# Kernel tuning notes

Measured on AMD Instinct MI355X. Metric: run time of the kernel, lower is better.

Reference implementation:

```python
import jax, jax.numpy as jnp
import numpy as np

DIM = 96       # d_model / channels
DSTATE = 16    # SSM state size N
DINNER = 2 * DIM   # expand=2 -> 192
DTRANK = 6     # ceil(DIM/16)
K = 4          # scan directions
B, H, W = 2, 56, 56


def _ln(x, g, b, eps=1e-5):
    m = x.mean(-1, keepdims=True)
    v = x.var(-1, keepdims=True)
    return (x - m) * jax.lax.rsqrt(v + eps) * g + b


def _dwconv3(x, w, b):  # x [B,C,H,W], w [C,1,3,3] depthwise, SAME padding
    y = jax.lax.conv_general_dilated(x, w, (1, 1), [(1, 1), (1, 1)],
                                     feature_group_count=x.shape[1],
                                     dimension_numbers=('NCHW', 'OIHW', 'NCHW'))
    return y + b[None, :, None, None]


def _bn(x, g, b, m, v, eps=1e-5):  # eval-mode BatchNorm2d on NCHW
    inv = jax.lax.rsqrt(v + eps)
    return (x - m[None, :, None, None]) * (inv * g)[None, :, None, None] + b[None, :, None, None]


def _selective_scan(u, dt, A, Bs, Cs, Dp, dt_bias):
    # u, dt: [B,K,D,L]; A: [K,D,N]; Bs,Cs: [B,K,N,L]; Dp, dt_bias: [K,D]
    dt = jax.nn.softplus(dt + dt_bias[None, :, :, None])
    dA = jnp.exp(jnp.einsum('bkdl,kdn->lbkdn', dt, A))           # [L,B,K,D,N]
    dBu = jnp.einsum('bkdl,bknl,bkdl->lbkdn', dt, Bs, u)          # [L,B,K,D,N]
    Ct = jnp.moveaxis(Cs, -1, 0)                                  # [L,B,K,N]
    h0 = jnp.zeros(dA.shape[1:], dA.dtype)

    def step(h, inp):
        dA_l, dBu_l, C_l = inp
        h = dA_l * h + dBu_l
        return h, jnp.einsum('bkdn,bkn->bkd', h, C_l)

    _, ys = jax.lax.scan(step, h0, (dA, dBu, Ct))                 # ys [L,B,K,D]
    return jnp.moveaxis(ys, 0, -1) + u * Dp[None, :, :, None]     # [B,K,D,L]


def setup_inputs() -> dict:
    key = jax.random.key(0)
    ks = jax.random.split(key, 12)
    s = 0.02
    f32 = jnp.float32
    inp = {}
    inp['x'] = jax.random.normal(ks[0], (B, H, W, DIM), f32)
    # conv branch: depthwise 3x3 + BN + ReLU + 1x1 + BN
    inp['dw_w'] = jax.random.normal(ks[1], (DIM, 1, 3, 3), f32) * s
    inp['dw_b'] = jnp.zeros((DIM,), f32)
    inp['bn1_g'] = jnp.ones((DIM,), f32); inp['bn1_b'] = jnp.zeros((DIM,), f32)
    inp['bn1_m'] = jnp.zeros((DIM,), f32); inp['bn1_v'] = jnp.ones((DIM,), f32)
    inp['pw_w'] = jax.random.normal(ks[2], (DIM, DIM), f32) * s
    inp['pw_b'] = jnp.zeros((DIM,), f32)
    inp['bn2_g'] = jnp.ones((DIM,), f32); inp['bn2_b'] = jnp.zeros((DIM,), f32)
    inp['bn2_m'] = jnp.zeros((DIM,), f32); inp['bn2_v'] = jnp.ones((DIM,), f32)
    # pre-mamba LayerNorm
    inp['ln_g'] = jnp.ones((DIM,), f32); inp['ln_b'] = jnp.zeros((DIM,), f32)
    # SS2D params
    inp['in_proj_w'] = jax.random.normal(ks[3], (2 * DINNER, DIM), f32) * s
    inp['conv_w'] = jax.random.normal(ks[4], (DINNER, 1, 3, 3), f32) * s
    inp['conv_b'] = jnp.zeros((DINNER,), f32)
    inp['x_proj_w'] = jax.random.normal(ks[5], (K, DTRANK + 2 * DSTATE, DINNER), f32) * s
    inp['dt_w'] = jax.random.normal(ks[6], (K, DINNER, DTRANK), f32) * s
    inp['dt_b'] = jnp.full((K, DINNER), -4.6, f32)  # softplus(dt_b) ~= 0.01
    inp['A_logs'] = jnp.log(jnp.tile(jnp.arange(1, DSTATE + 1, dtype=f32), (K * DINNER, 1)))
    inp['Ds'] = jnp.ones((K * DINNER,), f32)
    inp['out_norm_g'] = jnp.ones((DINNER,), f32); inp['out_norm_b'] = jnp.zeros((DINNER,), f32)
    inp['out_proj_w'] = jax.random.normal(ks[7], (DIM, DINNER), f32) * s
    # fusion: Linear(2*dim, dim) + LayerNorm(dim)
    inp['fus_w'] = jax.random.normal(ks[8], (DIM, 2 * DIM), f32) * s
    inp['fus_b'] = jnp.zeros((DIM,), f32)
    inp['fus_ln_g'] = jnp.ones((DIM,), f32); inp['fus_ln_b'] = jnp.zeros((DIM,), f32)
    return inp


def reference(x, dw_w, dw_b, bn1_g, bn1_b, bn1_m, bn1_v, pw_w, pw_b,
              bn2_g, bn2_b, bn2_m, bn2_v, ln_g, ln_b,
              in_proj_w, conv_w, conv_b, x_proj_w, dt_w, dt_b, A_logs, Ds,
              out_norm_g, out_norm_b, out_proj_w, fus_w, fus_b, fus_ln_g, fus_ln_b):
    Bsz, Hh, Ww, C = x.shape
    L = Hh * Ww
    # ----- conv branch -----
    xc = jnp.transpose(x, (0, 3, 1, 2))                       # [B,C,H,W]
    c = jax.nn.relu(_bn(_dwconv3(xc, dw_w, dw_b), bn1_g, bn1_b, bn1_m, bn1_v))
    c = jnp.einsum('bchw,oc->bohw', c, pw_w) + pw_b[None, :, None, None]
    conv_out = jnp.transpose(_bn(c, bn2_g, bn2_b, bn2_m, bn2_v), (0, 2, 3, 1))
    # ----- mamba (SS2D) branch -----
    xn = _ln(x, ln_g, ln_b)
    xz = xn @ in_proj_w.T                                     # [B,H,W,2*Din]
    xm, z = jnp.split(xz, 2, axis=-1)
    xm = jnp.transpose(xm, (0, 3, 1, 2))                      # [B,Din,H,W]
    xm = jax.nn.silu(_dwconv3(xm, conv_w, conv_b))
    v1 = xm.reshape(Bsz, DINNER, L)                           # row-major scan
    v2 = jnp.transpose(xm, (0, 1, 3, 2)).reshape(Bsz, DINNER, L)  # col-major scan
    xs = jnp.stack([v1, v2, v1[..., ::-1], v2[..., ::-1]], axis=1)  # [B,4,Din,L]
    x_dbl = jnp.einsum('bkdl,kcd->bkcl', xs, x_proj_w)
    dts, Bmat, Cmat = jnp.split(x_dbl, [DTRANK, DTRANK + DSTATE], axis=2)
    dts = jnp.einsum('bkrl,kdr->bkdl', dts, dt_w)
    A = -jnp.exp(A_logs).reshape(K, DINNER, DSTATE)
    out_y = _selective_scan(xs, dts, A, Bmat, Cmat, Ds.reshape(K, DINNER), dt_b)
    y1 = out_y[:, 0]
    inv_y = out_y[:, 2:4][..., ::-1]
    y2 = inv_y[:, 0]
    y3 = jnp.transpose(inv_y[:, 1].reshape(Bsz, DINNER, Ww, Hh), (0, 1, 3, 2)).reshape(Bsz, DINNER, L)
    y4 = jnp.transpose(out_y[:, 1].reshape(Bsz, DINNER, Ww, Hh), (0, 1, 3, 2)).reshape(Bsz, DINNER, L)
    y = jnp.transpose(y1 + y2 + y3 + y4, (0, 2, 1)).reshape(Bsz, Hh, Ww, DINNER)
    y = _ln(y, out_norm_g, out_norm_b)
    y = y * jax.nn.silu(z)
    mamba_out = y @ out_proj_w.T                              # [B,H,W,C]
    # ----- fusion + residual -----
    fused = jnp.concatenate([conv_out, mamba_out], axis=-1) @ fus_w.T + fus_b
    fused = _ln(fused, fus_ln_g, fus_ln_b)
    return x + fused
```

## Files before the change

kernel.cpp:

```cpp
#include <hip/hip_runtime.h>
#include <math.h>

#define BZ 2
#define HH 56
#define WW 56
#define LL 3136
#define CC 96
#define DI 192
#define NS 16
#define RR 6
#define NT 49
#define NCH 98
#define CH 32

#define OFF_CONV   0
#define OFF_XMRAW  602112
#define OFF_Z      1806336
#define OFF_V1     3010560
#define OFF_V2     4214784
#define OFF_DT     5419008
#define OFF_BS     10235904
#define OFF_CS     10637312
#define OFF_Y      11038720
#define OFF_Y13    15855616
#define OFF_T      18264064
#define OFF_W2     19468288

__device__ __forceinline__ float softplusf(float x) {
    if (x > 20.f) return x;
    return log1pf(__expf(x));
}

__global__ __launch_bounds__(64) void k0_w2(const float* __restrict__ fus_w,
                                            const float* __restrict__ opw,
                                            float* __restrict__ W2) {
    int i = blockIdx.x * 64 + threadIdx.x;
    if (i >= CC * DI) return;
    int o = i / DI, d = i % DI;
    float acc = 0.f;
    for (int j = 0; j < CC; ++j)
        acc += fus_w[o * DI + CC + j] * opw[j * DI + d];
    W2[i] = acc;
}

__global__ __launch_bounds__(256) void k0c_negA(const float* __restrict__ A_logs,
                                                float* __restrict__ negA) {
    int i = blockIdx.x * 256 + threadIdx.x;
    if (i < 4 * DI * NS) negA[i] = -__expf(A_logs[i]);
}

__global__ __launch_bounds__(256) void k1a_dw(const float* __restrict__ x,
    const float* __restrict__ dw_w, const float* __restrict__ dw_b,
    const float* __restrict__ bn1_g, const float* __restrict__ bn1_b,
    const float* __restrict__ bn1_m, const float* __restrict__ bn1_v,
    float* __restrict__ cbuf) {
    int i = blockIdx.x * 256 + threadIdx.x;
    if (i >= BZ * LL * CC) return;
    int c = i % CC;
    int bl = i / CC;
    int l = bl % LL, b = bl / LL;
    int h = l / WW, w = l % WW;
    float acc = dw_b[c];
    #pragma unroll
    for (int dy = -1; dy <= 1; ++dy) {
        int hh = h + dy; if (hh < 0 || hh >= HH) continue;
        #pragma unroll
        for (int dx = -1; dx <= 1; ++dx) {
            int ww = w + dx; if (ww < 0 || ww >= WW) continue;
            acc += x[((b * HH + hh) * WW + ww) * CC + c] * dw_w[c * 9 + (dy + 1) * 3 + (dx + 1)];
        }
    }
    float inv = rsqrtf(bn1_v[c] + 1e-5f);
    float v = (acc - bn1_m[c]) * inv * bn1_g[c] + bn1_b[c];
    cbuf[i] = fmaxf(v, 0.f);
}

__global__ __launch_bounds__(256) void k1b_pw(const float* __restrict__ cbuf,
    const float* __restrict__ pw_w, const float* __restrict__ pw_b,
    const float* __restrict__ bn2_g, const float* __restrict__ bn2_b,
    const float* __restrict__ bn2_m, const float* __restrict__ bn2_v,
    float* __restrict__ conv_out) {
    int t0 = blockIdx.x * 64;
    int og = blockIdx.y;
    int b = blockIdx.z;
    int lane = threadIdx.x & 63;
    int wvu = __builtin_amdgcn_readfirstlane(threadIdx.x >> 6);
    __shared__ float ct[CC * 65];
    __shared__ float res[64 * 49];
    const float* cb = cbuf + (b * LL + t0) * CC;
    for (int e = threadIdx.x; e < 64 * CC; e += 256) {
        int p = e / CC, c = e % CC;
        ct[c * 65 + p] = cb[e];
    }
    __syncthreads();
    int o0 = og * 48 + wvu * 12;
    float acc[12];
    const float* pb = pw_b + o0;
    #pragma unroll
    for (int j = 0; j < 12; ++j) acc[j] = pb[j];
    const float* wb = pw_w + o0 * CC;
    for (int c = 0; c < CC; ++c) {
        float xv = ct[c * 65 + lane];
        #pragma unroll
        for (int j = 0; j < 12; ++j)
            acc[j] += xv * wb[j * CC + c];
    }
    #pragma unroll
    for (int j = 0; j < 12; ++j) {
        int o = o0 + j;
        float inv = rsqrtf(bn2_v[o] + 1e-5f);
        res[lane * 49 + wvu * 12 + j] = (acc[j] - bn2_m[o]) * inv * bn2_g[o] + bn2_b[o];
    }
    __syncthreads();
    float* ob = conv_out + (b * LL + t0) * CC + og * 48;
    for (int e = threadIdx.x; e < 64 * 48; e += 256) {
        int pl = e / 48, o = e % 48;
        ob[pl * CC + o] = res[pl * 49 + o];
    }
}

__global__ __launch_bounds__(256) void k2_inproj(const float* __restrict__ x,
    const float* __restrict__ ln_g, const float* __restrict__ ln_b,
    const float* __restrict__ ipw,
    float* __restrict__ xm_raw, float* __restrict__ z_buf) {
    int t0 = blockIdx.x * 64;
    int og = blockIdx.y;
    int b = blockIdx.z;
    int lane = threadIdx.x & 63;
    int wv = threadIdx.x >> 6;
    int wvu = __builtin_amdgcn_readfirstlane(wv);
    __shared__ float xt[64 * 97];
    __shared__ float xn[96 * 65];
    __shared__ float ps[4][64], ps2[4][64];
    const float* xb = x + (b * LL + t0) * CC;
    for (int e = threadIdx.x; e < 64 * CC; e += 256) {
        int p = e / CC, c = e % CC;
        xt[p * 97 + c] = xb[e];
    }
    __syncthreads();
    float s = 0.f, s2 = 0.f;
    #pragma unroll
    for (int j = 0; j < 24; ++j) {
        float v = xt[lane * 97 + wvu * 24 + j];
        s += v; s2 += v * v;
    }
    ps[wv][lane] = s; ps2[wv][lane] = s2;
    __syncthreads();
    float st = 0.f, st2 = 0.f;
    #pragma unroll
    for (int i = 0; i < 4; ++i) { st += ps[i][lane]; st2 += ps2[i][lane]; }
    float m = st * (1.f / 96.f);
    float inv = rsqrtf(st2 * (1.f / 96.f) - m * m + 1e-5f);
    #pragma unroll
    for (int j = 0; j < 24; ++j) {
        int c = wvu * 24 + j;
        xn[c * 65 + lane] = (xt[lane * 97 + c] - m) * inv * ln_g[c] + ln_b[c];
    }
    __syncthreads();
    float acc[12];
    #pragma unroll
    for (int j = 0; j < 12; ++j) acc[j] = 0.f;
    int o0 = og * 48 + wvu * 12;
    const float* wbase = ipw + o0 * CC;
    for (int c = 0; c < CC; ++c) {
        float xv = xn[c * 65 + lane];
        #pragma unroll
        for (int j = 0; j < 12; ++j)
            acc[j] += xv * wbase[j * CC + c];
    }
    int p = t0 + lane;
    #pragma unroll
    for (int j = 0; j < 12; ++j) {
        int out = o0 + j;
        if (out < DI) xm_raw[(b * DI + out) * LL + p] = acc[j];
        else          z_buf[(b * DI + (out - DI)) * LL + p] = acc[j];
    }
}

__global__ __launch_bounds__(256) void k3_dw(const float* __restrict__ xm_raw,
    const float* __restrict__ conv_w, const float* __restrict__ conv_b,
    float* __restrict__ v1, float* __restrict__ v2) {
    int bd = blockIdx.x;
    int half = blockIdx.y;
    int d = bd % DI;
    int h0 = half * 28;
    __shared__ float tile[28 * 57];
    const float* src = xm_raw + bd * LL;
    float wloc[9];
    #pragma unroll
    for (int i = 0; i < 9; ++i) wloc[i] = conv_w[d * 9 + i];
    float bias = conv_b[d];
    for (int e = threadIdx.x; e < 28 * WW; e += 256) {
        int hl = e / WW, w = e % WW;
        int h = h0 + hl;
        float acc = bias;
        #pragma unroll
        for (int dy = -1; dy <= 1; ++dy) {
            int hh = h + dy; if (hh < 0 || hh >= HH) continue;
            #pragma unroll
            for (int dx = -1; dx <= 1; ++dx) {
                int ww = w + dx; if (ww < 0 || ww >= WW) continue;
                acc += src[hh * WW + ww] * wloc[(dy + 1) * 3 + (dx + 1)];
            }
        }
        float sig = 1.f / (1.f + __expf(-acc));
        float v = acc * sig;
        v1[bd * LL + h * WW + w] = v;
        tile[hl * 57 + w] = v;
    }
    __syncthreads();
    for (int e = threadIdx.x; e < 28 * WW; e += 256) {
        int w = e / 28, hl = e % 28;
        v2[bd * LL + w * HH + h0 + hl] = tile[hl * 57 + w];
    }
}

__global__ __launch_bounds__(256) void k4a_xproj(const float* __restrict__ v1,
    const float* __restrict__ v2, const float* __restrict__ xpw,
    float* __restrict__ dtr_g, float* __restrict__ B_s, float* __restrict__ C_s) {
    int tile = blockIdx.x;
    int k = blockIdx.y, b = blockIdx.z;
    int lane = threadIdx.x & 63;
    int wvu = __builtin_amdgcn_readfirstlane(threadIdx.x >> 6);
    int t0 = tile * 64;
    int r0 = wvu * 10; if (r0 > 28) r0 = 28;
    const float* src = ((k & 1) == 0 ? v1 : v2) + b * DI * LL + t0;
    float acc[10];
    #pragma unroll
    for (int i = 0; i < 10; ++i) acc[i] = 0.f;
    const float* wbase = xpw + (k * 38 + r0) * DI;
    for (int d = 0; d < DI; ++d) {
        float xv = src[d * LL + lane];
        #pragma unroll
        for (int i = 0; i < 10; ++i)
            acc[i] += xv * wbase[i * DI + d];
    }
    int bk = b * 4 + k;
    int p = t0 + lane;
    #pragma unroll
    for (int i = 0; i < 10; ++i) {
        int c = r0 + i;
        if (c < RR) {
            dtr_g[(bk * RR + c) * LL + p] = acc[i];
        } else if (c < RR + NS) {
            B_s[(bk * NS + (c - RR)) * LL + p] = acc[i];
        } else {
            C_s[(bk * NS + (c - RR - NS)) * LL + p] = acc[i];
        }
    }
}

__global__ __launch_bounds__(256) void k4b_dt(const float* __restrict__ dtr_g,
    const float* __restrict__ dtw, const float* __restrict__ dtb,
    float* __restrict__ dt_s) {
    int t0 = blockIdx.x * 64;
    int k = blockIdx.y, b = blockIdx.z;
    int lane = threadIdx.x & 63;
    int wvu = __builtin_amdgcn_readfirstlane(threadIdx.x >> 6);
    int bk = b * 4 + k;
    int p = t0 + lane;
    float r[RR];
    #pragma unroll
    for (int i = 0; i < RR; ++i) r[i] = dtr_g[(bk * RR + i) * LL + p];
    for (int i = 0; i < 48; ++i) {
        int d = wvu * 48 + i;
        float a = dtb[k * DI + d];
        const float* wr = dtw + (k * DI + d) * RR;
        #pragma unroll
        for (int q = 0; q < RR; ++q)
            a += r[q] * wr[q];
        dt_s[(bk * DI + d) * LL + p] = softplusf(a);
    }
}

__global__ __launch_bounds__(128, 4) void k5a_scan(const float* __restrict__ dt_s,
    const float* __restrict__ B_s, const float* __restrict__ C_s,
    const float* __restrict__ v1, const float* __restrict__ v2,
    const float* __restrict__ A_logs, float* __restrict__ y_scan,
    float* __restrict__ hl_buf, float* __restrict__ Tbuf) {
    int bx = blockIdx.x;
    int dg = bx % 3, c = bx / 3;
    int k = blockIdx.y, b = blockIdx.z;
    int bk = b * 4 + k;
    int tid = threadIdx.x;
    int lane = tid & 63;
    int wvu = __builtin_amdgcn_readfirstlane(tid >> 6);
    int d0 = dg * 64, d = d0 + lane;
    bool fwd = (k < 2);
    int s0 = fwd ? c * CH : (LL - (c + 1) * CH);
    __shared__ float dtl[64 * 32];
    __shared__ float ul[64 * 32];
    __shared__ alignas(16) float bc[32 * 32];
    float Ae[8];
    const float* ap = A_logs + (k * DI + d) * NS + wvu * 8;
    #pragma unroll
    for (int n = 0; n < 8; ++n) Ae[n] = -__expf(ap[n]) * 1.442695040888963f;
    const float* dtp = dt_s + (bk * DI + d0) * LL + s0;
    const float* up  = ((k & 1) == 0 ? v1 : v2) + (b * DI + d0) * LL + s0;
    #pragma unroll
    for (int q = 0; q < 4; ++q) {
        int e = q * 128 + tid;
        int row = e >> 3;
        int p4 = (e & 7) << 2;
        float4 dv = *(const float4*)(dtp + row * LL + p4);
        float4 uv = *(const float4*)(up + row * LL + p4);
        float dvv[4] = {dv.x, dv.y, dv.z, dv.w};
        float uvv[4] = {uv.x, uv.y, uv.z, uv.w};
        int rsw = row & 31;
        #pragma unroll
        for (int t = 0; t < 4; ++t) {
            int s = fwd ? (p4 + t) : (31 - (p4 + t));
            dtl[row * 32 + (s ^ rsw)] = dvv[t];
            ul [row * 32 + (s ^ rsw)] = dvv[t] * uvv[t];
        }
    }
    #pragma unroll
    for (int q = 0; q < 2; ++q) {
        int e = q * 128 + tid;
        int row = e >> 3;
        int p4 = (e & 7) << 2;
        const float* src = (row < 16 ? B_s + (bk * NS + row) * LL
                                     : C_s + (bk * NS + (row - 16)) * LL) + s0 + p4;
        float4 v = *(const float4*)src;
        float vv[4] = {v.x, v.y, v.z, v.w};
        #pragma unroll
        for (int t = 0; t < 4; ++t) {
            int s = fwd ? (p4 + t) : (31 - (p4 + t));
            bc[s * 32 + (row ^ ((s & 7) << 2))] = vv[t];
        }
    }
    __syncthreads();
    float h[8];
    #pragma unroll
    for (int n = 0; n < 8; ++n) h[n] = 0.f;
    float cum = 0.f;
    int lbase = lane * 32;
    int lsw = lane & 31;
    int w8 = wvu * 8;
    #pragma unroll
    for (int seg = 0; seg < 4; ++seg) {
        float yv_[8];
        #pragma unroll
        for (int jj = 0; jj < 8; ++jj) {
            int j = seg * 8 + jj;
            float dtv = dtl[lbase + (j ^ lsw)];
            float du  = ul [lbase + (j ^ lsw)];
            cum += dtv;
            int cswz = (j & 7) << 2;
            const float* rb0 = &bc[j * 32 + ( w8       ^ cswz)];
            const float* rb1 = &bc[j * 32 + ((w8 +  4) ^ cswz)];
            const float* rc0 = &bc[j * 32 + ((w8 + 16) ^ cswz)];
            const float* rc1 = &bc[j * 32 + ((w8 + 20) ^ cswz)];
            float4 b0 = *(const float4*)rb0, b1 = *(const float4*)rb1;
            float4 c0 = *(const float4*)rc0, c1 = *(const float4*)rc1;
            float bv[8] = {b0.x, b0.y, b0.z, b0.w, b1.x, b1.y, b1.z, b1.w};
            float cv[8] = {c0.x, c0.y, c0.z, c0.w, c1.x, c1.y, c1.z, c1.w};
            float y = 0.f;
            #pragma unroll
            for (int n = 0; n < 8; ++n) {
                h[n] = exp2f(dtv * Ae[n]) * h[n] + du * bv[n];
                y += h[n] * cv[n];
            }
            yv_[jj] = y;
        }
        __syncthreads();
        float* dst = (wvu == 0) ? dtl : ul;
        #pragma unroll
        for (int jj = 0; jj < 8; ++jj) {
            int j = seg * 8 + jj;
            dst[lbase + (j ^ lsw)] = yv_[jj];
        }
    }
    __syncthreads();
    float* yp = y_scan + (bk * DI + d0) * LL + s0;
    #pragma unroll
    for (int q = 0; q < 4; ++q) {
        int e = q * 128 + tid;
        int row = e >> 3;
        int p4 = (e & 7) << 2;
        int rsw = row & 31;
        float ov[4];
        #pragma unroll
        for (int t = 0; t < 4; ++t) {
            int s = fwd ? (p4 + t) : (31 - (p4 + t));
            ov[t] = dtl[row * 32 + (s ^ rsw)] + ul[row * 32 + (s ^ rsw)];
        }
        *(float4*)(yp + row * LL + p4) = make_float4(ov[0], ov[1], ov[2], ov[3]);
    }
    float4* hp4 = (float4*)(hl_buf + (bk * NCH + c) * (DI * NS) + d * NS + wvu * 8);
    hp4[0] = make_float4(h[0], h[1], h[2], h[3]);
    hp4[1] = make_float4(h[4], h[5], h[6], h[7]);
    if (wvu == 0) Tbuf[(bk * NCH + c) * DI + d] = cum;
}

__global__ __launch_bounds__(64) void k5c_comb(float* __restrict__ hl_buf,
    const float* __restrict__ Tbuf, const float* __restrict__ negA) {
    int dg = blockIdx.x, k = blockIdx.y, b = blockIdx.z;
    int lane = threadIdx.x, dl = lane >> 4, n = lane & 15;
    int d = dg * 4 + dl;
    int bk = b * 4 + k;
    float Av = negA[(k * DI + d) * NS + n];
    float H = 0.f;
    float* slot0 = hl_buf + (bk * NCH + 0) * (DI * NS) + dg * 64 + lane;
    float hl_next = *slot0;
    float T_next = Tbuf[(bk * NCH + 0) * DI + d];
    for (int c = 0; c < NCH; ++c) {
        float hl = hl_next, T = T_next;
        if (c + 1 < NCH) {
            hl_next = hl_buf[(bk * NCH + c + 1) * (DI * NS) + dg * 64 + lane];
            T_next  = Tbuf[(bk * NCH + c + 1) * DI + d];
        }
        hl_buf[(bk * NCH + c) * (DI * NS) + dg * 64 + lane] = H;
        H = hl + __expf(Av * T) * H;
    }
}

__global__ __launch_bounds__(256) void k5d_corr(const float* __restrict__ dt_s,
    const float* __restrict__ C_s, const float* __restrict__ hin,
    const float* __restrict__ negA, float* __restrict__ y_scan) {
    int t = blockIdx.x;
    int k = blockIdx.y, b = blockIdx.z;
    bool fwd = (k < 2);
    int c  = fwd ? (t + 1) : (NCH - 1 - t);
    int s0 = fwd ? (t + 1) * CH : t * CH;
    int p32 = threadIdx.x & 31, sl = threadIdx.x >> 5;
    int bk = b * 4 + k;
    __shared__ float c_l[16 * 33];
    for (int e = threadIdx.x; e < 16 * CH; e += 256) {
        int n = e >> 5, s = e & 31;
        c_l[n * 33 + s] = C_s[(bk * NS + n) * LL + s0 + s];
    }
    __syncthreads();
    for (int j = 0; j < 24; ++j) {
        int d = sl * 24 + j;
        float dtv = dt_s[(bk * DI + d) * LL + s0 + p32];
        float cum = dtv;
        if (fwd) {
            #pragma unroll
            for (int off = 1; off < 32; off <<= 1) {
                float o = __shfl_up(cum, off, 32);
                if (p32 >= off) cum += o;
            }
        } else {
            #pragma unroll
            for (int off = 1; off < 32; off <<= 1) {
                float o = __shfl_down(cum, off, 32);
                if (p32 < 32 - off) cum += o;
            }
        }
        const float* hp = hin + (bk * NCH + c) * (DI * NS) + d * 16;
        const float* ap = negA + (k * DI + d) * NS;
        float acc = 0.f;
        #pragma unroll
        for (int n = 0; n < 16; ++n) {
            acc += c_l[n * 33 + p32] * __expf(ap[n] * cum) * hp[n];
        }
        y_scan[(bk * DI + d) * LL + s0 + p32] += acc;
    }
}

__global__ __launch_bounds__(256) void k5b_tr(const float* __restrict__ y_scan,
                                              float* __restrict__ y13t) {
    int idx = blockIdx.x;
    int d = idx % DI;
    int bk = idx / DI;
    int kk = bk % 2, b = bk / 2;
    int k = (kk == 0) ? 1 : 3;
    __shared__ float tile[HH * 57];
    const float* src = y_scan + ((b * 4 + k) * DI + d) * LL;
    for (int e = threadIdx.x; e < LL; e += 256) {
        int w = e / HH, h = e % HH;
        tile[h * 57 + w] = src[e];
    }
    __syncthreads();
    float* dst = y13t + idx * LL;
    for (int e = threadIdx.x; e < LL; e += 256) {
        int h = e / WW, w = e % WW;
        dst[e] = tile[h * 57 + w];
    }
}

__global__ __launch_bounds__(256) void k6_gather(const float* __restrict__ y_scan,
    const float* __restrict__ y13t, const float* __restrict__ v1,
    const float* __restrict__ z_buf, const float* __restrict__ Ds,
    const float* __restrict__ ong, const float* __restrict__ onb,
    float* __restrict__ t_buf) {
    int t0 = blockIdx.x * 16;
    int b = blockIdx.y;
    int p16 = threadIdx.x & 15, sl = threadIdx.x >> 4;
    int p = t0 + p16;
    __shared__ float yv[DI * 17];
    __shared__ float ps[16][16], ps2[16][16];
    float s = 0.f, s2 = 0.f;
    for (int j = 0; j < 12; ++j) {
        int d = sl * 12 + j;
        float dsum = Ds[d] + Ds[DI + d] + Ds[2 * DI + d] + Ds[3 * DI + d];
        float val = y_scan[((b * 4 + 0) * DI + d) * LL + p]
                  + y_scan[((b * 4 + 2) * DI + d) * LL + p]
                  + y13t[((b * 2 + 0) * DI + d) * LL + p]
                  + y13t[((b * 2 + 1) * DI + d) * LL + p]
                  + v1[(b * DI + d) * LL + p] * dsum;
        yv[d * 17 + p16] = val;
        s += val; s2 += val * val;
    }
    ps[sl][p16] = s; ps2[sl][p16] = s2;
    __syncthreads();
    float st = 0.f, st2 = 0.f;
    #pragma unroll
    for (int i = 0; i < 16; ++i) { st += ps[i][p16]; st2 += ps2[i][p16]; }
    float m = st * (1.f / 192.f);
    float inv = rsqrtf(st2 * (1.f / 192.f) - m * m + 1e-5f);
    for (int j = 0; j < 12; ++j) {
        int d = sl * 12 + j;
        float val = (yv[d * 17 + p16] - m) * inv * ong[d] + onb[d];
        float zz = z_buf[(b * DI + d) * LL + p];
        float sig = 1.f / (1.f + __expf(-zz));
        t_buf[(b * DI + d) * LL + p] = val * zz * sig;
    }
}

__global__ __launch_bounds__(256) void k7a_mm(const float* __restrict__ t_buf,
    const float* __restrict__ conv_out, const float* __restrict__ W2,
    const float* __restrict__ fus_w, const float* __restrict__ fus_b,
    float* __restrict__ fusedT) {
    int t0 = blockIdx.x * 64;
    int og = blockIdx.y;
    int b = blockIdx.z;
    int lane = threadIdx.x & 63;
    int wvu = __builtin_amdgcn_readfirstlane(threadIdx.x >> 6);
    __shared__ float ct[CC * 65];
    const float* cb = conv_out + (b * LL + t0) * CC;
    for (int e = threadIdx.x; e < 64 * CC; e += 256) {
        int p = e / CC, c = e % CC;
        ct[c * 65 + p] = cb[e];
    }
    __syncthreads();
    int o0 = og * 12 + wvu * 3;
    float acc[3];
    #pragma unroll
    for (int j = 0; j < 3; ++j) acc[j] = fus_b[o0 + j];
    int p = t0 + lane;
    const float* w2 = W2 + o0 * DI;
    for (int d = 0; d < DI; ++d) {
        float tv = t_buf[(b * DI + d) * LL + p];
        #pragma unroll
        for (int j = 0; j < 3; ++j)
            acc[j] += tv * w2[j * DI + d];
    }
    const float* fw = fus_w + o0 * DI;
    for (int c = 0; c < CC; ++c) {
        float cv = ct[c * 65 + lane];
        #pragma unroll
        for (int j = 0; j < 3; ++j)
            acc[j] += cv * fw[j * DI + c];
    }
    #pragma unroll
    for (int j = 0; j < 3; ++j)
        fusedT[(b * CC + o0 + j) * LL + p] = acc[j];
}

__global__ __launch_bounds__(256) void k7b_ln(const float* __restrict__ fusedT,
    const float* __restrict__ flg, const float* __restrict__ flb,
    const float* __restrict__ x, float* __restrict__ out) {
    int t0 = blockIdx.x * 16;
    int b = blockIdx.y;
    int p16 = threadIdx.x & 15, sl = threadIdx.x >> 4;
    __shared__ float ft[CC * 17];
    __shared__ float res[16 * 97];
    __shared__ float ps[16][16], ps2[16][16];
    for (int e = threadIdx.x; e < CC * 16; e += 256) {
        int o = e >> 4, p = e & 15;
        ft[o * 17 + p] = fusedT[(b * CC + o) * LL + t0 + p];
    }
    __syncthreads();
    float s = 0.f, s2 = 0.f;
    #pragma unroll
    for (int j = 0; j < 6; ++j) {
        float v = ft[(sl * 6 + j) * 17 + p16];
        s += v; s2 += v * v;
    }
    ps[sl][p16] = s; ps2[sl][p16] = s2;
    __syncthreads();
    float st = 0.f, st2 = 0.f;
    #pragma unroll
    for (int i = 0; i < 16; ++i) { st += ps[i][p16]; st2 += ps2[i][p16]; }
    float m = st * (1.f / 96.f);
    float inv = rsqrtf(st2 * (1.f / 96.f) - m * m + 1e-5f);
    #pragma unroll
    for (int j = 0; j < 6; ++j) {
        int o = sl * 6 + j;
        res[p16 * 97 + o] = (ft[o * 17 + p16] - m) * inv * flg[o] + flb[o];
    }
    __syncthreads();
    const float* xb = x + (b * LL + t0) * CC;
    float* ob = out + (b * LL + t0) * CC;
    for (int e = threadIdx.x; e < 16 * CC; e += 256) {
        int pl = e / CC, o = e % CC;
        ob[e] = xb[e] + res[pl * 97 + o];
    }
}

extern "C" void kernel_launch(void* const* d_in, const int* in_sizes, int n_in,
                              void* d_out, int out_size, void* d_ws, size_t ws_size,
                              hipStream_t stream) {
    const float* x        = (const float*)d_in[0];
    const float* dw_w     = (const float*)d_in[1];
    const float* dw_b     = (const float*)d_in[2];
    const float* bn1_g    = (const float*)d_in[3];
    const float* bn1_b    = (const float*)d_in[4];
    const float* bn1_m    = (const float*)d_in[5];
    const float* bn1_v    = (const float*)d_in[6];
    const float* pw_w     = (const float*)d_in[7];
    const float* pw_b     = (const float*)d_in[8];
    const float* bn2_g    = (const float*)d_in[9];
    const float* bn2_b    = (const float*)d_in[10];
    const float* bn2_m    = (const float*)d_in[11];
    const float* bn2_v    = (const float*)d_in[12];
    const float* ln_g     = (const float*)d_in[13];
    const float* ln_b     = (const float*)d_in[14];
    const float* ipw      = (const float*)d_in[15];
    const float* conv_w   = (const float*)d_in[16];
    const float* conv_b   = (const float*)d_in[17];
    const float* xpw      = (const float*)d_in[18];
    const float* dtw      = (const float*)d_in[19];
    const float* dtb      = (const float*)d_in[20];
    const float* A_logs   = (const float*)d_in[21];
    const float* Ds       = (const float*)d_in[22];
    const float* ong      = (const float*)d_in[23];
    const float* onb      = (const float*)d_in[24];
    const float* opw      = (const float*)d_in[25];
    const float* fus_w    = (const float*)d_in[26];
    const float* fus_b    = (const float*)d_in[27];
    const float* flg      = (const float*)d_in[28];
    const float* flb      = (const float*)d_in[29];

    float* ws = (float*)d_ws;
    float* conv_out = ws + OFF_CONV;
    float* xm_raw   = ws + OFF_XMRAW;
    float* z_buf    = ws + OFF_Z;
    float* v1       = ws + OFF_V1;
    float* v2       = ws + OFF_V2;
    float* dt_s     = ws + OFF_DT;
    float* B_s      = ws + OFF_BS;
    float* C_s      = ws + OFF_CS;
    float* y_scan   = ws + OFF_Y;
    float* y13t     = ws + OFF_Y13;
    float* t_buf    = ws + OFF_T;
    float* W2       = ws + OFF_W2;
    float* cbuf     = y13t;
    float* hl_buf   = y13t;
    float* Tbuf     = xm_raw;
    float* dtr_g    = xm_raw + 262144;
    float* negA     = B_s;
    float* fusedT   = y13t;
    float* out      = (float*)d_out;

    k0_w2<<<dim3((CC * DI + 63) / 64), dim3(64), 0, stream>>>(fus_w, opw, W2);
    k1a_dw<<<dim3((BZ * LL * CC + 255) / 256), dim3(256), 0, stream>>>(x, dw_w, dw_b,
                                                     bn1_g, bn1_b, bn1_m, bn1_v, cbuf);
    k1b_pw<<<dim3(NT, 2, BZ), dim3(256), 0, stream>>>(cbuf, pw_w, pw_b,
                                                   bn2_g, bn2_b, bn2_m, bn2_v, conv_out);
    k2_inproj<<<dim3(NT, 8, BZ), dim3(256), 0, stream>>>(x, ln_g, ln_b, ipw, xm_raw, z_buf);
    k3_dw<<<dim3(BZ * DI, 2), dim3(256), 0, stream>>>(xm_raw, conv_w, conv_b, v1, v2);
    k4a_xproj<<<dim3(NT, 4, BZ), dim3(256), 0, stream>>>(v1, v2, xpw, dtr_g, B_s, C_s);
    k4b_dt<<<dim3(NT, 4, BZ), dim3(256), 0, stream>>>(dtr_g, dtw, dtb, dt_s);
    k5a_scan<<<dim3(3 * NCH, 4, BZ), dim3(128), 0, stream>>>(dt_s, B_s, C_s, v1, v2, A_logs,
                                                             y_scan, hl_buf, Tbuf);
    k0c_negA<<<dim3(48), dim3(256), 0, stream>>>(A_logs, negA);
    k5c_comb<<<dim3(48, 4, BZ), dim3(64), 0, stream>>>(hl_buf, Tbuf, negA);
    k5d_corr<<<dim3(NCH - 1, 4, BZ), dim3(256), 0, stream>>>(dt_s, C_s, hl_buf, negA, y_scan);
    k5b_tr<<<dim3(BZ * 2 * DI), dim3(256), 0, stream>>>(y_scan, y13t);
    k6_gather<<<dim3(196, BZ), dim3(256), 0, stream>>>(y_scan, y13t, v1, z_buf, Ds, ong, onb, t_buf);
    k7a_mm<<<dim3(NT, 8, BZ), dim3(256), 0, stream>>>(t_buf, conv_out, W2, fus_w, fus_b, fusedT);
    k7b_ln<<<dim3(196, BZ), dim3(256), 0, stream>>>(fusedT, flg, flb, x, out);
}
```

Baseline: 357.2 us.

## Fuse dt projection and softplus into scan and correction kernels

Removes the separate dt kernel and its 2x4x192x3136 dt_s buffer. The scan and correction kernels now rebuild dt from the rank-6 projection on the fly (6 FMAs plus softplus per element), cutting a large global write and two reads. The combine kernel also gains an 8-deep software prefetch of chunk states to hide load latency on its serial chain. The cost is that dt is computed twice, and the scan kernel's prologue carries more arithmetic and register pressure.

```diff
diff --git a/kernel.cpp b/kernel.cpp
--- a/kernel.cpp
+++ b/kernel.cpp
@@ -250,30 +250,8 @@
     }
 }
 
-__global__ __launch_bounds__(256) void k4b_dt(const float* __restrict__ dtr_g,
+__global__ __launch_bounds__(128, 4) void k5a_scan(const float* __restrict__ dtr_g,
     const float* __restrict__ dtw, const float* __restrict__ dtb,
-    float* __restrict__ dt_s) {
-    int t0 = blockIdx.x * 64;
-    int k = blockIdx.y, b = blockIdx.z;
-    int lane = threadIdx.x & 63;
-    int wvu = __builtin_amdgcn_readfirstlane(threadIdx.x >> 6);
-    int bk = b * 4 + k;
-    int p = t0 + lane;
-    float r[RR];
-    #pragma unroll
-    for (int i = 0; i < RR; ++i) r[i] = dtr_g[(bk * RR + i) * LL + p];
-    for (int i = 0; i < 48; ++i) {
-        int d = wvu * 48 + i;
-        float a = dtb[k * DI + d];
-        const float* wr = dtw + (k * DI + d) * RR;
-        #pragma unroll
-        for (int q = 0; q < RR; ++q)
-            a += r[q] * wr[q];
-        dt_s[(bk * DI + d) * LL + p] = softplusf(a);
-    }
-}
-
-__global__ __launch_bounds__(128, 4) void k5a_scan(const float* __restrict__ dt_s,
     const float* __restrict__ B_s, const float* __restrict__ C_s,
     const float* __restrict__ v1, const float* __restrict__ v2,
     const float* __restrict__ A_logs, float* __restrict__ y_scan,
@@ -291,44 +269,62 @@
     __shared__ float dtl[64 * 32];
     __shared__ float ul[64 * 32];
     __shared__ alignas(16) float bc[32 * 32];
-    float Ae[8];
-    const float* ap = A_logs + (k * DI + d) * NS + wvu * 8;
-    #pragma unroll
-    for (int n = 0; n < 8; ++n) Ae[n] = -__expf(ap[n]) * 1.442695040888963f;
-    const float* dtp = dt_s + (bk * DI + d0) * LL + s0;
     const float* up  = ((k & 1) == 0 ? v1 : v2) + (b * DI + d0) * LL + s0;
+    int p4 = (tid & 7) << 2;
+    int row0 = tid >> 3;
+    const float* dtrp = dtr_g + (bk * RR) * LL + s0 + p4;
+    float4 rv0 = *(const float4*)(dtrp + 0 * LL);
+    float4 rv1 = *(const float4*)(dtrp + 1 * LL);
+    float4 rv2 = *(const float4*)(dtrp + 2 * LL);
+    float4 rv3 = *(const float4*)(dtrp + 3 * LL);
+    float4 rv4 = *(const float4*)(dtrp + 4 * LL);
+    float4 rv5 = *(const float4*)(dtrp + 5 * LL);
     #pragma unroll
     for (int q = 0; q < 4; ++q) {
-        int e = q * 128 + tid;
-        int row = e >> 3;
-        int p4 = (e & 7) << 2;
-        float4 dv = *(const float4*)(dtp + row * LL + p4);
+        int row = row0 + 16 * q;
+        int dd = k * DI + d0 + row;
+        const float* wr = dtw + dd * RR;
+        float2 w01 = *(const float2*)(wr);
+        float2 w23 = *(const float2*)(wr + 2);
+        float2 w45 = *(const float2*)(wr + 4);
+        float bias = dtb[dd];
+        float a0 = bias, a1 = bias, a2 = bias, a3 = bias;
+        a0 += rv0.x * w01.x; a1 += rv0.y * w01.x; a2 += rv0.z * w01.x; a3 += rv0.w * w01.x;
+        a0 += rv1.x * w01.y; a1 += rv1.y * w01.y; a2 += rv1.z * w01.y; a3 += rv1.w * w01.y;
+        a0 += rv2.x * w23.x; a1 += rv2.y * w23.x; a2 += rv2.z * w23.x; a3 += rv2.w * w23.x;
+        a0 += rv3.x * w23.y; a1 += rv3.y * w23.y; a2 += rv3.z * w23.y; a3 += rv3.w * w23.y;
+        a0 += rv4.x * w45.x; a1 += rv4.y * w45.x; a2 += rv4.z * w45.x; a3 += rv4.w * w45.x;
+        a0 += rv5.x * w45.y; a1 += rv5.y * w45.y; a2 += rv5.z * w45.y; a3 += rv5.w * w45.y;
+        float dts[4] = {softplusf(a0), softplusf(a1), softplusf(a2), softplusf(a3)};
         float4 uv = *(const float4*)(up + row * LL + p4);
-        float dvv[4] = {dv.x, dv.y, dv.z, dv.w};
         float uvv[4] = {uv.x, uv.y, uv.z, uv.w};
         int rsw = row & 31;
         #pragma unroll
         for (int t = 0; t < 4; ++t) {
             int s = fwd ? (p4 + t) : (31 - (p4 + t));
-            dtl[row * 32 + (s ^ rsw)] = dvv[t];
-            ul [row * 32 + (s ^ rsw)] = dvv[t] * uvv[t];
+            dtl[row * 32 + (s ^ rsw)] = dts[t];
+            ul [row * 32 + (s ^ rsw)] = dts[t] * uvv[t];
         }
     }
     #pragma unroll
     for (int q = 0; q < 2; ++q) {
         int e = q * 128 + tid;
         int row = e >> 3;
-        int p4 = (e & 7) << 2;
+        int pp4 = (e & 7) << 2;
         const float* src = (row < 16 ? B_s + (bk * NS + row) * LL
-                                     : C_s + (bk * NS + (row - 16)) * LL) + s0 + p4;
+                                     : C_s + (bk * NS + (row - 16)) * LL) + s0 + pp4;
         float4 v = *(const float4*)src;
         float vv[4] = {v.x, v.y, v.z, v.w};
         #pragma unroll
         for (int t = 0; t < 4; ++t) {
-            int s = fwd ? (p4 + t) : (31 - (p4 + t));
+            int s = fwd ? (pp4 + t) : (31 - (pp4 + t));
             bc[s * 32 + (row ^ ((s & 7) << 2))] = vv[t];
         }
     }
+    float Ae[8];
+    const float* ap = A_logs + (k * DI + d) * NS + wvu * 8;
+    #pragma unroll
+    for (int n = 0; n < 8; ++n) Ae[n] = -__expf(ap[n]) * 1.442695040888963f;
     __syncthreads();
     float h[8];
     #pragma unroll
@@ -377,15 +373,15 @@
     for (int q = 0; q < 4; ++q) {
         int e = q * 128 + tid;
         int row = e >> 3;
-        int p4 = (e & 7) << 2;
+        int pp4 = (e & 7) << 2;
         int rsw = row & 31;
         float ov[4];
         #pragma unroll
         for (int t = 0; t < 4; ++t) {
-            int s = fwd ? (p4 + t) : (31 - (p4 + t));
+            int s = fwd ? (pp4 + t) : (31 - (pp4 + t));
             ov[t] = dtl[row * 32 + (s ^ rsw)] + ul[row * 32 + (s ^ rsw)];
         }
-        *(float4*)(yp + row * LL + p4) = make_float4(ov[0], ov[1], ov[2], ov[3]);
+        *(float4*)(yp + row * LL + pp4) = make_float4(ov[0], ov[1], ov[2], ov[3]);
     }
     float4* hp4 = (float4*)(hl_buf + (bk * NCH + c) * (DI * NS) + d * NS + wvu * 8);
     hp4[0] = make_float4(h[0], h[1], h[2], h[3]);
@@ -399,23 +395,32 @@
     int lane = threadIdx.x, dl = lane >> 4, n = lane & 15;
     int d = dg * 4 + dl;
     int bk = b * 4 + k;
+    const int HS = DI * NS;
     float Av = negA[(k * DI + d) * NS + n];
+    float* hp = hl_buf + (bk * NCH) * HS + dg * 64 + lane;
+    const float* Tp = Tbuf + (bk * NCH) * DI + d;
+    float hl[8], T[8];
+    #pragma unroll
+    for (int i = 0; i < 8; ++i) { hl[i] = hp[i * HS]; T[i] = Tp[i * DI]; }
     float H = 0.f;
-    float* slot0 = hl_buf + (bk * NCH + 0) * (DI * NS) + dg * 64 + lane;
-    float hl_next = *slot0;
-    float T_next = Tbuf[(bk * NCH + 0) * DI + d];
-    for (int c = 0; c < NCH; ++c) {
-        float hl = hl_next, T = T_next;
-        if (c + 1 < NCH) {
-            hl_next = hl_buf[(bk * NCH + c + 1) * (DI * NS) + dg * 64 + lane];
-            T_next  = Tbuf[(bk * NCH + c + 1) * DI + d];
-        }
-        hl_buf[(bk * NCH + c) * (DI * NS) + dg * 64 + lane] = H;
-        H = hl + __expf(Av * T) * H;
-    }
-}
-
-__global__ __launch_bounds__(256) void k5d_corr(const float* __restrict__ dt_s,
+    for (int cb = 0; cb < 96; cb += 8) {
+        #pragma unroll
+        for (int i = 0; i < 8; ++i) {
+            int c = cb + i;
+            float hlv = hl[i], Tv = T[i];
+            int nc = c + 8;
+            if (nc < NCH) { hl[i] = hp[nc * HS]; T[i] = Tp[nc * DI]; }
+            hp[c * HS] = H;
+            H = hlv + __expf(Av * Tv) * H;
+        }
+    }
+    hp[96 * HS] = H;
+    H = hl[0] + __expf(Av * T[0]) * H;
+    hp[97 * HS] = H;
+}
+
+__global__ __launch_bounds__(256) void k5d_corr(const float* __restrict__ dtr_g,
+    const float* __restrict__ dtw, const float* __restrict__ dtb,
     const float* __restrict__ C_s, const float* __restrict__ hin,
     const float* __restrict__ negA, float* __restrict__ y_scan) {
     int t = blockIdx.x;
@@ -430,10 +435,20 @@
         int n = e >> 5, s = e & 31;
         c_l[n * 33 + s] = C_s[(bk * NS + n) * LL + s0 + s];
     }
+    const float* rp = dtr_g + (bk * RR) * LL + s0 + p32;
+    float r[RR];
+    #pragma unroll
+    for (int q = 0; q < RR; ++q) r[q] = rp[q * LL];
     __syncthreads();
     for (int j = 0; j < 24; ++j) {
         int d = sl * 24 + j;
-        float dtv = dt_s[(bk * DI + d) * LL + s0 + p32];
+        int dd = k * DI + d;
+        const float* wr = dtw + dd * RR;
+        float a = dtb[dd];
+        #pragma unroll
+        for (int q = 0; q < RR; ++q)
+            a += r[q] * wr[q];
+        float dtv = softplusf(a);
         float cum = dtv;
         if (fwd) {
             #pragma unroll
@@ -640,7 +655,6 @@
     float* z_buf    = ws + OFF_Z;
     float* v1       = ws + OFF_V1;
     float* v2       = ws + OFF_V2;
-    float* dt_s     = ws + OFF_DT;
     float* B_s      = ws + OFF_BS;
     float* C_s      = ws + OFF_CS;
     float* y_scan   = ws + OFF_Y;
@@ -663,12 +677,13 @@
     k2_inproj<<<dim3(NT, 8, BZ), dim3(256), 0, stream>>>(x, ln_g, ln_b, ipw, xm_raw, z_buf);
     k3_dw<<<dim3(BZ * DI, 2), dim3(256), 0, stream>>>(xm_raw, conv_w, conv_b, v1, v2);
     k4a_xproj<<<dim3(NT, 4, BZ), dim3(256), 0, stream>>>(v1, v2, xpw, dtr_g, B_s, C_s);
-    k4b_dt<<<dim3(NT, 4, BZ), dim3(256), 0, stream>>>(dtr_g, dtw, dtb, dt_s);
-    k5a_scan<<<dim3(3 * NCH, 4, BZ), dim3(128), 0, stream>>>(dt_s, B_s, C_s, v1, v2, A_logs,
+    k5a_scan<<<dim3(3 * NCH, 4, BZ), dim3(128), 0, stream>>>(dtr_g, dtw, dtb, B_s, C_s,
+                                                             v1, v2, A_logs,
                                                              y_scan, hl_buf, Tbuf);
     k0c_negA<<<dim3(48), dim3(256), 0, stream>>>(A_logs, negA);
     k5c_comb<<<dim3(48, 4, BZ), dim3(64), 0, stream>>>(hl_buf, Tbuf, negA);
-    k5d_corr<<<dim3(NCH - 1, 4, BZ), dim3(256), 0, stream>>>(dt_s, C_s, hl_buf, negA, y_scan);
+    k5d_corr<<<dim3(NCH - 1, 4, BZ), dim3(256), 0, stream>>>(dtr_g, dtw, dtb, C_s,
+                                                             hl_buf, negA, y_scan);
     k5b_tr<<<dim3(BZ * 2 * DI), dim3(256), 0, stream>>>(y_scan, y13t);
     k6_gather<<<dim3(196, BZ), dim3(256), 0, stream>>>(y_scan, y13t, v1, z_buf, Ds, ong, onb, t_buf);
     k7a_mm<<<dim3(NT, 8, BZ), dim3(256), 0, stream>>>(t_buf, conv_out, W2, fus_w, fus_b, fusedT);
```

New measurement: 353.5 us. No clear change (-1.0%).
